# Performance work log

Measured on AMD Instinct MI355X. Metric: run time of the kernel, lower is better.

## Reference

```python
import jax, jax.numpy as jnp
import numpy as np

EMBED = 512
HEADS = 8
HEAD_DIM = EMBED // HEADS
N, S = 4, 2048


def setup_inputs() -> dict:
    key = jax.random.key(0)
    ks = jax.random.split(key, 10)
    value = jax.random.normal(ks[0], (N, S, EMBED), dtype=jnp.float32)
    k_in = jax.random.normal(ks[1], (N, S, EMBED), dtype=jnp.float32)
    q_in = jax.random.normal(ks[2], (N, S, EMBED), dtype=jnp.float32)
    mask = jax.random.randint(ks[3], (N, 1, S, S), 0, 2, dtype=jnp.int32)
    s = 1.0 / np.sqrt(HEAD_DIM)
    Wq = jax.random.uniform(ks[4], (HEAD_DIM, HEAD_DIM), minval=-s, maxval=s, dtype=jnp.float32)
    Wk = jax.random.uniform(ks[5], (HEAD_DIM, HEAD_DIM), minval=-s, maxval=s, dtype=jnp.float32)
    Wv = jax.random.uniform(ks[6], (HEAD_DIM, HEAD_DIM), minval=-s, maxval=s, dtype=jnp.float32)
    so = 1.0 / np.sqrt(EMBED)
    Wo = jax.random.uniform(ks[7], (EMBED, EMBED), minval=-so, maxval=so, dtype=jnp.float32)
    bo = jax.random.uniform(ks[8], (EMBED,), minval=-so, maxval=so, dtype=jnp.float32)
    return {"value": value, "key": k_in, "query": q_in, "mask": mask,
            "Wq": Wq, "Wk": Wk, "Wv": Wv, "Wo": Wo, "bo": bo}


def reference(value, key, query, mask, Wq, Wk, Wv, Wo, bo):
    n, qlen = query.shape[0], query.shape[1]
    # split heads: (N, L, H, D)
    v = value.reshape(n, -1, HEADS, HEAD_DIM)
    k = key.reshape(n, -1, HEADS, HEAD_DIM)
    q = query.reshape(n, qlen, HEADS, HEAD_DIM)
    # per-head linear projections (torch Linear: x @ W^T, no bias)
    v = jnp.einsum('nlhd,ed->nlhe', v, Wv)
    k = jnp.einsum('nlhd,ed->nlhe', k, Wk)
    q = jnp.einsum('nqhd,ed->nqhe', q, Wq)
    # energy: (N, H, Q, K)
    energy = jnp.einsum('nqhd,nkhd->nhqk', q, k)
    energy = jnp.where(mask == 0, jnp.float32(-1e20), energy)
    # NOTE: original scales by sqrt(embed_size), not sqrt(head_dim)
    attn = jax.nn.softmax(energy / jnp.sqrt(jnp.float32(EMBED)), axis=3)
    out = jnp.einsum('nhql,nlhd->nqhd', attn, v).reshape(n, qlen, EMBED)
    return out @ Wo.T + bo
```

## Files before the change

kernel.cpp:

```cpp
#include <hip/hip_runtime.h>

typedef short short8 __attribute__((ext_vector_type(8)));
typedef float f32x4 __attribute__((ext_vector_type(4)));
typedef unsigned short ushort4v __attribute__((ext_vector_type(4)));
typedef unsigned long long u64;
typedef u64 u64x2 __attribute__((ext_vector_type(2)));

#define N_B   4
#define S_LEN 2048
#define EMB   512
#define HD    64
#define NHB   32
#define QSCALE 0.04419417382415922f

__device__ unsigned short g_Wqb[64*64];
__device__ unsigned short g_Wkb[64*64];
__device__ unsigned short g_Wvb[64*64];
__device__ unsigned short g_Wob[512*512];
__device__ unsigned short g_Qp[NHB*S_LEN*HD];
__device__ unsigned short g_Kp[NHB*S_LEN*HD];
__device__ unsigned short g_Vt[NHB*HD*S_LEN];
__device__ unsigned short g_AO[N_B*S_LEN*EMB];
__device__ u64            g_Mb[N_B*32*S_LEN];

__device__ __forceinline__ unsigned short f2bf(float f) {
  unsigned u = __float_as_uint(f);
  u = u + 0x7fffu + ((u >> 16) & 1u);
  return (unsigned short)(u >> 16);
}

__global__ __launch_bounds__(256) void k0_wconv(const float* __restrict__ Wq,
                                                const float* __restrict__ Wk,
                                                const float* __restrict__ Wv,
                                                const float* __restrict__ Wo) {
  int idx = blockIdx.x * 256 + threadIdx.x;
  if (idx < 4096)        g_Wqb[idx]         = f2bf(Wq[idx] * QSCALE);
  else if (idx < 8192)   g_Wkb[idx - 4096]  = f2bf(Wk[idx - 4096]);
  else if (idx < 12288)  g_Wvb[idx - 8192]  = f2bf(Wv[idx - 8192]);
  else                   g_Wob[idx - 12288] = f2bf(Wo[idx - 12288]);
}

__global__ __launch_bounds__(256) void k0b_mask(const int* __restrict__ mask) {
  int wid = blockIdx.x * 4 + (threadIdx.x >> 6);
  int lane = threadIdx.x & 63;
  int q = wid & 2047;
  int nt = wid >> 11;
  int t = nt & 31, n = nt >> 5;
  int mk = mask[((size_t)(n * 2048 + q) << 11) + t * 64 + lane];
  u64 bits = __ballot(mk != 0);
  if (lane == 0) g_Mb[wid] = bits;
}

__global__ __launch_bounds__(256) void k1_proj(const float* __restrict__ q_in,
                                               const float* __restrict__ k_in,
                                               const float* __restrict__ v_in) {
  const int tid = threadIdx.x;
  const int w = tid >> 6, lane = tid & 63, g = lane >> 4, c = lane & 15;
  const int s0 = blockIdx.x * 64;
  const int nh = blockIdx.y, n = nh >> 3, h = nh & 7;
  const int which = blockIdx.z;
  const float* src = which == 0 ? q_in : (which == 1 ? k_in : v_in);
  const unsigned short* Wb = which == 0 ? g_Wqb : (which == 1 ? g_Wkb : g_Wvb);

  short8 xb[2];
  const int srow = s0 + w * 16 + c;
#pragma unroll
  for (int ks = 0; ks < 2; ++ks) {
    const float* ap = src + ((size_t)n * S_LEN + srow) * EMB + h * HD + ks * 32 + g * 8;
    f32x4 x0 = *(const f32x4*)ap;
    f32x4 x1 = *(const f32x4*)(ap + 4);
    short8 tt;
    tt[0] = (short)f2bf(x0[0]); tt[1] = (short)f2bf(x0[1]);
    tt[2] = (short)f2bf(x0[2]); tt[3] = (short)f2bf(x0[3]);
    tt[4] = (short)f2bf(x1[0]); tt[5] = (short)f2bf(x1[1]);
    tt[6] = (short)f2bf(x1[2]); tt[7] = (short)f2bf(x1[3]);
    xb[ks] = tt;
  }

  f32x4 acc[4];
#pragma unroll
  for (int dt = 0; dt < 4; ++dt) { acc[dt][0]=0.f; acc[dt][1]=0.f; acc[dt][2]=0.f; acc[dt][3]=0.f; }

#pragma unroll
  for (int ks = 0; ks < 2; ++ks)
#pragma unroll
    for (int dt = 0; dt < 4; ++dt) {
      short8 a = *(const short8*)(Wb + (dt * 16 + c) * HD + ks * 32 + g * 8);
      acc[dt] = __builtin_amdgcn_mfma_f32_16x16x32_bf16(a, xb[ks], acc[dt], 0, 0, 0);
    }

  if (which < 2) {
    unsigned short* dst = which == 0 ? g_Qp : g_Kp;
#pragma unroll
    for (int dt = 0; dt < 4; ++dt) {
      ushort4v u;
      u[0] = f2bf(acc[dt][0]); u[1] = f2bf(acc[dt][1]);
      u[2] = f2bf(acc[dt][2]); u[3] = f2bf(acc[dt][3]);
      *(ushort4v*)(dst + ((size_t)nh * S_LEN + srow) * HD + dt * 16 + 4 * g) = u;
    }
  } else {
#pragma unroll
    for (int dt = 0; dt < 4; ++dt)
#pragma unroll
      for (int r = 0; r < 4; ++r)
        g_Vt[((size_t)nh * HD + dt * 16 + 4 * g + r) * S_LEN + srow] = f2bf(acc[dt][r]);
  }
}

__global__ __launch_bounds__(512) void k2_attn() {
  __shared__ unsigned short Kl[2][64][64];
  __shared__ unsigned short Vl[2][64][64];
  __shared__ unsigned short Pl[8][16][64];
  const int tid = threadIdx.x;
  const int w = tid >> 6, lane = tid & 63, g = lane >> 4, c = lane & 15;
  const int q0 = blockIdx.x * 128;
  const int nh = blockIdx.y, n = nh >> 3, h = nh & 7;

  short8 aq[2];
#pragma unroll
  for (int ks = 0; ks < 2; ++ks)
    aq[ks] = *(const short8*)(g_Qp + ((size_t)nh * S_LEN + q0 + w * 16 + c) * HD + ks * 32 + g * 8);

  const int strow = tid >> 3, schunk = tid & 7;
  const int sdst = (schunk ^ (strow & 7)) * 8;
  const unsigned short* ksrc = g_Kp + ((size_t)nh * S_LEN + strow) * HD + schunk * 8;
  const unsigned short* vsrc = g_Vt + ((size_t)nh * HD + strow) * S_LEN + schunk * 8;
  const u64* mbase = g_Mb + ((size_t)n * 32) * S_LEN + q0 + w * 16 + 4 * g;

  float m4[4], l4[4];
  f32x4 O4[4];
#pragma unroll
  for (int r = 0; r < 4; ++r) { m4[r] = -1e29f; l4[r] = 0.f; }
#pragma unroll
  for (int dt = 0; dt < 4; ++dt) { O4[dt][0]=0.f; O4[dt][1]=0.f; O4[dt][2]=0.f; O4[dt][3]=0.f; }

  short8 kst = *(const short8*)(ksrc);
  short8 vst = *(const short8*)(vsrc);
  u64x2 mA = *(const u64x2*)(mbase);
  u64x2 mB = *(const u64x2*)(mbase + 2);
  *(short8*)(&Kl[0][strow][sdst]) = kst;
  *(short8*)(&Vl[0][strow][sdst]) = vst;
  __syncthreads();

  for (int t = 0; t < 32; ++t) {
    const int cur = t & 1;
    u64x2 mAn, mBn;
    if (t < 31) {
      kst = *(const short8*)(ksrc + (size_t)(t + 1) * 64 * HD);
      vst = *(const short8*)(vsrc + (t + 1) * 64);
      mAn = *(const u64x2*)(mbase + (size_t)(t + 1) * S_LEN);
      mBn = *(const u64x2*)(mbase + (size_t)(t + 1) * S_LEN + 2);
    }

    f32x4 sa[4];
#pragma unroll
    for (int ct = 0; ct < 4; ++ct) { sa[ct][0]=0.f; sa[ct][1]=0.f; sa[ct][2]=0.f; sa[ct][3]=0.f; }
#pragma unroll
    for (int ks = 0; ks < 2; ++ks)
#pragma unroll
      for (int ct = 0; ct < 4; ++ct) {
        short8 bk = *(const short8*)(&Kl[cur][ct * 16 + c][((g + 4 * ks) ^ (c & 7)) * 8]);
        sa[ct] = __builtin_amdgcn_mfma_f32_16x16x32_bf16(aq[ks], bk, sa[ct], 0, 0, 0);
      }

#pragma unroll
    for (int r = 0; r < 4; ++r) {
      u64 m64 = (r == 0) ? mA[0] : (r == 1) ? mA[1] : (r == 2) ? mB[0] : mB[1];
      unsigned lo = (unsigned)m64, hi = (unsigned)(m64 >> 32);
#pragma unroll
      for (int ct = 0; ct < 4; ++ct) {
        unsigned word = (ct & 2) ? hi : lo;
        int sh = (ct & 1) * 16 + c;
        sa[ct][r] = ((word >> sh) & 1u) ? sa[ct][r] : -1e30f;
      }
    }

    float corr[4];
#pragma unroll
    for (int r = 0; r < 4; ++r) {
      float mx = fmaxf(fmaxf(sa[0][r], sa[1][r]), fmaxf(sa[2][r], sa[3][r]));
      mx = fmaxf(mx, __shfl_xor(mx, 1));
      mx = fmaxf(mx, __shfl_xor(mx, 2));
      mx = fmaxf(mx, __shfl_xor(mx, 4));
      mx = fmaxf(mx, __shfl_xor(mx, 8));
      float mn = fmaxf(m4[r], mx);
      corr[r] = __expf(m4[r] - mn);
      m4[r] = mn;
      float ps = 0.f;
#pragma unroll
      for (int ct = 0; ct < 4; ++ct) {
        float p = __expf(sa[ct][r] - mn);
        sa[ct][r] = p;
        ps += p;
      }
      ps += __shfl_xor(ps, 1); ps += __shfl_xor(ps, 2);
      ps += __shfl_xor(ps, 4); ps += __shfl_xor(ps, 8);
      l4[r] = l4[r] * corr[r] + ps;
    }

#pragma unroll
    for (int ct = 0; ct < 4; ++ct)
#pragma unroll
      for (int r = 0; r < 4; ++r) {
        int prow = 4 * g + r, col = ct * 16 + c;
        Pl[w][prow][(((col >> 3) ^ (prow & 7)) << 3) | (col & 7)] = f2bf(sa[ct][r]);
      }

#pragma unroll
    for (int dt = 0; dt < 4; ++dt)
#pragma unroll
      for (int r = 0; r < 4; ++r)
        O4[dt][r] *= corr[r];

#pragma unroll
    for (int ks = 0; ks < 2; ++ks) {
      short8 pa = *(const short8*)(&Pl[w][c][((g + 4 * ks) ^ (c & 7)) * 8]);
#pragma unroll
      for (int dt = 0; dt < 4; ++dt) {
        short8 bv = *(const short8*)(&Vl[cur][dt * 16 + c][((g + 4 * ks) ^ (c & 7)) * 8]);
        O4[dt] = __builtin_amdgcn_mfma_f32_16x16x32_bf16(pa, bv, O4[dt], 0, 0, 0);
      }
    }

    __syncthreads();
    if (t < 31) {
      *(short8*)(&Kl[cur ^ 1][strow][sdst]) = kst;
      *(short8*)(&Vl[cur ^ 1][strow][sdst]) = vst;
      mA = mAn; mB = mBn;
    }
    __syncthreads();
  }

#pragma unroll
  for (int r = 0; r < 4; ++r) {
    float inv = l4[r] > 0.f ? 1.f / l4[r] : 0.f;
    int qr = q0 + w * 16 + 4 * g + r;
#pragma unroll
    for (int dt = 0; dt < 4; ++dt)
      g_AO[((size_t)n * S_LEN + qr) * EMB + h * HD + dt * 16 + c] = f2bf(O4[dt][r] * inv);
  }
}

__global__ __launch_bounds__(256) void k3_oproj(const float* __restrict__ bo,
                                                float* __restrict__ out) {
  const int tid = threadIdx.x;
  const int w = tid >> 6, lane = tid & 63, g = lane >> 4, c = lane & 15;
  const int m0 = blockIdx.x * 64;
  const int n0 = blockIdx.y * 64;

  f32x4 acc[4];
#pragma unroll
  for (int ct = 0; ct < 4; ++ct) { acc[ct][0]=0.f; acc[ct][1]=0.f; acc[ct][2]=0.f; acc[ct][3]=0.f; }

  for (int ks = 0; ks < 16; ++ks) {
    short8 a = *(const short8*)(g_AO + ((size_t)(m0 + w * 16 + c)) * EMB + ks * 32 + g * 8);
#pragma unroll
    for (int ct = 0; ct < 4; ++ct) {
      short8 b = *(const short8*)(g_Wob + (size_t)(n0 + ct * 16 + c) * EMB + ks * 32 + g * 8);
      acc[ct] = __builtin_amdgcn_mfma_f32_16x16x32_bf16(a, b, acc[ct], 0, 0, 0);
    }
  }

#pragma unroll
  for (int ct = 0; ct < 4; ++ct) {
    int col = n0 + ct * 16 + c;
    float bias = bo[col];
#pragma unroll
    for (int r = 0; r < 4; ++r) {
      int row = m0 + w * 16 + 4 * g + r;
      out[(size_t)row * EMB + col] = acc[ct][r] + bias;
    }
  }
}

extern "C" void kernel_launch(void* const* d_in, const int* in_sizes, int n_in,
                              void* d_out, int out_size, void* d_ws, size_t ws_size,
                              hipStream_t stream) {
  const float* value = (const float*)d_in[0];
  const float* key   = (const float*)d_in[1];
  const float* query = (const float*)d_in[2];
  const int*   mask  = (const int*)d_in[3];
  const float* Wq    = (const float*)d_in[4];
  const float* Wk    = (const float*)d_in[5];
  const float* Wv    = (const float*)d_in[6];
  const float* Wo    = (const float*)d_in[7];
  const float* bo    = (const float*)d_in[8];
  float* out = (float*)d_out;

  k0_wconv<<<1072, 256, 0, stream>>>(Wq, Wk, Wv, Wo);
  k0b_mask<<<65536, 256, 0, stream>>>(mask);
  k1_proj<<<dim3(32, 32, 3), 256, 0, stream>>>(query, key, value);
  k2_attn<<<dim3(16, 32), 512, 0, stream>>>();
  k3_oproj<<<dim3(128, 8), 256, 0, stream>>>(bo, out);
}
```

Before: 326.3 us.

## Drop online-softmax max tracking, fold row sums into MFMA, coalesce mask and Vt writes

The attention kernel no longer tracks a running max or rescales the output. It folds log2(e) into the Q scale, computes exp2 directly, and zeroes masked entries. The row sums come from an extra MFMA against a block of ones appended to the V tile in shared memory, and bf16 packing uses v_cvt_pk_bf16_f32. One of the two barriers per tile is removed. Separately, the mask-packing kernel loops over 32 tiles per wave, and the V projection stages its transpose in LDS so the global stores are coalesced. Skipping the max subtraction risks exp overflow when scores are large, so correctness depends on the scores staying within a bounded range.

```diff
diff --git a/kernel.cpp b/kernel.cpp
--- a/kernel.cpp
+++ b/kernel.cpp
@@ -11,7 +11,9 @@
 #define EMB   512
 #define HD    64
 #define NHB   32
-#define QSCALE 0.04419417382415922f
+#define QSCALE 0.063758714f
+
+#define EXP2F(x) __builtin_amdgcn_exp2f(x)
 
 __device__ unsigned short g_Wqb[64*64];
 __device__ unsigned short g_Wkb[64*64];
@@ -29,6 +31,12 @@
   return (unsigned short)(u >> 16);
 }
 
+__device__ __forceinline__ unsigned cvt_pk_bf16(float a, float b) {
+  unsigned r;
+  asm("v_cvt_pk_bf16_f32 %0, %1, %2" : "=v"(r) : "v"(a), "v"(b));
+  return r;
+}
+
 __global__ __launch_bounds__(256) void k0_wconv(const float* __restrict__ Wq,
                                                 const float* __restrict__ Wk,
                                                 const float* __restrict__ Wv,
@@ -43,17 +51,21 @@
 __global__ __launch_bounds__(256) void k0b_mask(const int* __restrict__ mask) {
   int wid = blockIdx.x * 4 + (threadIdx.x >> 6);
   int lane = threadIdx.x & 63;
-  int q = wid & 2047;
-  int nt = wid >> 11;
-  int t = nt & 31, n = nt >> 5;
-  int mk = mask[((size_t)(n * 2048 + q) << 11) + t * 64 + lane];
-  u64 bits = __ballot(mk != 0);
-  if (lane == 0) g_Mb[wid] = bits;
+  int n = wid >> 11, q = wid & 2047;
+  const int* base = mask + ((size_t)(n * 2048 + q) << 11);
+  u64* dst = g_Mb + (size_t)n * 32 * S_LEN + q;
+#pragma unroll 4
+  for (int j = 0; j < 32; ++j) {
+    int mk = base[j * 64 + lane];
+    u64 bits = __ballot(mk != 0);
+    if (lane == 0) dst[(size_t)j * S_LEN] = bits;
+  }
 }
 
 __global__ __launch_bounds__(256) void k1_proj(const float* __restrict__ q_in,
                                                const float* __restrict__ k_in,
                                                const float* __restrict__ v_in) {
+  __shared__ unsigned short VtL[64][72];
   const int tid = threadIdx.x;
   const int w = tid >> 6, lane = tid & 63, g = lane >> 4, c = lane & 15;
   const int s0 = blockIdx.x * 64;
@@ -103,18 +115,26 @@
     for (int dt = 0; dt < 4; ++dt)
 #pragma unroll
       for (int r = 0; r < 4; ++r)
-        g_Vt[((size_t)nh * HD + dt * 16 + 4 * g + r) * S_LEN + srow] = f2bf(acc[dt][r]);
+        VtL[dt * 16 + 4 * g + r][w * 16 + c] = f2bf(acc[dt][r]);
+    __syncthreads();
+#pragma unroll
+    for (int rep = 0; rep < 2; ++rep) {
+      int cid = tid + rep * 256;
+      int row = cid >> 3, ch = cid & 7;
+      short8 v = *(const short8*)(&VtL[row][ch * 8]);
+      *(short8*)(g_Vt + ((size_t)nh * HD + row) * S_LEN + s0 + ch * 8) = v;
+    }
   }
 }
 
 __global__ __launch_bounds__(512) void k2_attn() {
   __shared__ unsigned short Kl[2][64][64];
-  __shared__ unsigned short Vl[2][64][64];
+  __shared__ unsigned short Vl[2][80][64];
   __shared__ unsigned short Pl[8][16][64];
   const int tid = threadIdx.x;
   const int w = tid >> 6, lane = tid & 63, g = lane >> 4, c = lane & 15;
   const int q0 = blockIdx.x * 128;
-  const int nh = blockIdx.y, n = nh >> 3, h = nh & 7;
+  const int nh = blockIdx.y, n = nh >> 3;
 
   short8 aq[2];
 #pragma unroll
@@ -127,12 +147,17 @@
   const unsigned short* vsrc = g_Vt + ((size_t)nh * HD + strow) * S_LEN + schunk * 8;
   const u64* mbase = g_Mb + ((size_t)n * 32) * S_LEN + q0 + w * 16 + 4 * g;
 
-  float m4[4], l4[4];
-  f32x4 O4[4];
-#pragma unroll
-  for (int r = 0; r < 4; ++r) { m4[r] = -1e29f; l4[r] = 0.f; }
+  {
+    int flat = tid * 4;
+    int b = flat >> 10, rem = flat & 1023, rr = rem >> 6, cc = rem & 63;
+    ushort4v ones4 = {0x3f80, 0x3f80, 0x3f80, 0x3f80};
+    *(ushort4v*)(&Vl[b][64 + rr][cc]) = ones4;
+  }
+
+  f32x4 O4[4], O5;
 #pragma unroll
   for (int dt = 0; dt < 4; ++dt) { O4[dt][0]=0.f; O4[dt][1]=0.f; O4[dt][2]=0.f; O4[dt][3]=0.f; }
+  O5[0]=0.f; O5[1]=0.f; O5[2]=0.f; O5[3]=0.f;
 
   short8 kst = *(const short8*)(ksrc);
   short8 vst = *(const short8*)(vsrc);
@@ -163,77 +188,55 @@
         sa[ct] = __builtin_amdgcn_mfma_f32_16x16x32_bf16(aq[ks], bk, sa[ct], 0, 0, 0);
       }
 
-#pragma unroll
-    for (int r = 0; r < 4; ++r) {
-      u64 m64 = (r == 0) ? mA[0] : (r == 1) ? mA[1] : (r == 2) ? mB[0] : mB[1];
-      unsigned lo = (unsigned)m64, hi = (unsigned)(m64 >> 32);
-#pragma unroll
-      for (int ct = 0; ct < 4; ++ct) {
-        unsigned word = (ct & 2) ? hi : lo;
-        int sh = (ct & 1) * 16 + c;
-        sa[ct][r] = ((word >> sh) & 1u) ? sa[ct][r] : -1e30f;
+    unsigned lo0 = (unsigned)mA[0], hi0 = (unsigned)(mA[0] >> 32);
+    unsigned lo1 = (unsigned)mA[1], hi1 = (unsigned)(mA[1] >> 32);
+    unsigned lo2 = (unsigned)mB[0], hi2 = (unsigned)(mB[0] >> 32);
+    unsigned lo3 = (unsigned)mB[1], hi3 = (unsigned)(mB[1] >> 32);
+#pragma unroll
+    for (int ct = 0; ct < 4; ++ct) {
+      const int sh = (ct & 1) * 16 + c;
+      float p0 = ((((ct & 2) ? hi0 : lo0) >> sh) & 1u) ? EXP2F(sa[ct][0]) : 0.f;
+      float p1 = ((((ct & 2) ? hi1 : lo1) >> sh) & 1u) ? EXP2F(sa[ct][1]) : 0.f;
+      float p2 = ((((ct & 2) ? hi2 : lo2) >> sh) & 1u) ? EXP2F(sa[ct][2]) : 0.f;
+      float p3 = ((((ct & 2) ? hi3 : lo3) >> sh) & 1u) ? EXP2F(sa[ct][3]) : 0.f;
+      unsigned pk01 = cvt_pk_bf16(p0, p1);
+      unsigned pk23 = cvt_pk_bf16(p2, p3);
+      const int col = ct * 16 + c;
+      const int chs = ((col >> 3) << 3);
+#pragma unroll
+      for (int r = 0; r < 4; ++r) {
+        int prow = 4 * g + r;
+        unsigned pk = (r < 2) ? pk01 : pk23;
+        unsigned short v = (r & 1) ? (unsigned short)(pk >> 16) : (unsigned short)pk;
+        Pl[w][prow][(chs ^ ((prow & 7) << 3)) | (col & 7)] = v;
       }
     }
-
-    float corr[4];
-#pragma unroll
-    for (int r = 0; r < 4; ++r) {
-      float mx = fmaxf(fmaxf(sa[0][r], sa[1][r]), fmaxf(sa[2][r], sa[3][r]));
-      mx = fmaxf(mx, __shfl_xor(mx, 1));
-      mx = fmaxf(mx, __shfl_xor(mx, 2));
-      mx = fmaxf(mx, __shfl_xor(mx, 4));
-      mx = fmaxf(mx, __shfl_xor(mx, 8));
-      float mn = fmaxf(m4[r], mx);
-      corr[r] = __expf(m4[r] - mn);
-      m4[r] = mn;
-      float ps = 0.f;
-#pragma unroll
-      for (int ct = 0; ct < 4; ++ct) {
-        float p = __expf(sa[ct][r] - mn);
-        sa[ct][r] = p;
-        ps += p;
-      }
-      ps += __shfl_xor(ps, 1); ps += __shfl_xor(ps, 2);
-      ps += __shfl_xor(ps, 4); ps += __shfl_xor(ps, 8);
-      l4[r] = l4[r] * corr[r] + ps;
-    }
-
-#pragma unroll
-    for (int ct = 0; ct < 4; ++ct)
-#pragma unroll
-      for (int r = 0; r < 4; ++r) {
-        int prow = 4 * g + r, col = ct * 16 + c;
-        Pl[w][prow][(((col >> 3) ^ (prow & 7)) << 3) | (col & 7)] = f2bf(sa[ct][r]);
-      }
-
-#pragma unroll
-    for (int dt = 0; dt < 4; ++dt)
-#pragma unroll
-      for (int r = 0; r < 4; ++r)
-        O4[dt][r] *= corr[r];
 
 #pragma unroll
     for (int ks = 0; ks < 2; ++ks) {
       short8 pa = *(const short8*)(&Pl[w][c][((g + 4 * ks) ^ (c & 7)) * 8]);
 #pragma unroll
-      for (int dt = 0; dt < 4; ++dt) {
+      for (int dt = 0; dt < 5; ++dt) {
         short8 bv = *(const short8*)(&Vl[cur][dt * 16 + c][((g + 4 * ks) ^ (c & 7)) * 8]);
-        O4[dt] = __builtin_amdgcn_mfma_f32_16x16x32_bf16(pa, bv, O4[dt], 0, 0, 0);
+        if (dt < 4)
+          O4[dt] = __builtin_amdgcn_mfma_f32_16x16x32_bf16(pa, bv, O4[dt], 0, 0, 0);
+        else
+          O5 = __builtin_amdgcn_mfma_f32_16x16x32_bf16(pa, bv, O5, 0, 0, 0);
       }
     }
 
-    __syncthreads();
     if (t < 31) {
       *(short8*)(&Kl[cur ^ 1][strow][sdst]) = kst;
       *(short8*)(&Vl[cur ^ 1][strow][sdst]) = vst;
       mA = mAn; mB = mBn;
-    }
-    __syncthreads();
-  }
-
+      __syncthreads();
+    }
+  }
+
+  const int h = nh & 7;
 #pragma unroll
   for (int r = 0; r < 4; ++r) {
-    float inv = l4[r] > 0.f ? 1.f / l4[r] : 0.f;
+    float inv = O5[r] > 0.f ? 1.f / O5[r] : 0.f;
     int qr = q0 + w * 16 + 4 * g + r;
 #pragma unroll
     for (int dt = 0; dt < 4; ++dt)
@@ -288,7 +291,7 @@
   float* out = (float*)d_out;
 
   k0_wconv<<<1072, 256, 0, stream>>>(Wq, Wk, Wv, Wo);
-  k0b_mask<<<65536, 256, 0, stream>>>(mask);
+  k0b_mask<<<2048, 256, 0, stream>>>(mask);
   k1_proj<<<dim3(32, 32, 3), 256, 0, stream>>>(query, key, value);
   k2_attn<<<dim3(16, 32), 512, 0, stream>>>();
   k3_oproj<<<dim3(128, 8), 256, 0, stream>>>(bo, out);
```

New measurement: 273.4 us. -16.2%, faster.
